# Performance work log

Hardware: AMD Instinct MI355X
Metric: run time of the kernel (lower is better)

## Reference

```python
import jax, jax.numpy as jnp
import numpy as np

HEADS = 8
SCALE_BASE = 512
EPS = 1e-5


def xpos(x, downscale=False):
    # x: (B, h, S, hd) ; XPOS rotary embedding with exponential scale
    hd = x.shape[-1]
    S = x.shape[-2]
    half = hd // 2
    base_scale = (jnp.arange(0, hd, 2, dtype=jnp.float32) + 0.4 * hd) / (1.4 * hd)  # (half,)
    pos = jnp.arange(S, dtype=jnp.float32)
    scale = base_scale[None, :] ** (pos[:, None] / SCALE_BASE)  # (S, half)
    inv_freq = 1.0 / (10000.0 ** (jnp.arange(half, dtype=jnp.float32) / half))
    sinu = pos[:, None] * inv_freq[None, :]  # (S, half)
    sin, cos = jnp.sin(sinu), jnp.cos(sinu)
    if downscale:
        scale = 1.0 / scale
    # duplicate_interleave: (S, half) -> (S, hd)
    sin_s = jnp.repeat(sin * scale, 2, axis=-1)
    cos_s = jnp.repeat(cos * scale, 2, axis=-1)
    x1 = x[..., ::2]
    x2 = x[..., 1::2]
    rot = jnp.stack((-x2, x1), axis=-1).reshape(x.shape)  # rotate_every_two
    return x * cos_s + rot * sin_s


def decay_mask(S):
    # (heads, S, S): gamma^(n-m) for n>=m else 0
    gammas = 1.0 - jnp.exp(jnp.linspace(np.log(1 / 32), np.log(1 / 512), HEADS)).astype(jnp.float32)
    n = jnp.arange(S, dtype=jnp.float32)
    diff = n[:, None] - n[None, :]
    lg = jnp.log(gammas)[:, None, None]
    return jnp.where(diff >= 0, jnp.exp(jnp.maximum(diff, 0.0) * lg), 0.0)


def layer_norm(x, w, b):
    mu = x.mean(-1, keepdims=True)
    var = x.var(-1, keepdims=True)
    return (x - mu) / jnp.sqrt(var + EPS) * w + b


def multiscale_retention(Xq, Xkv, Wq, Wk, Wv, Wg, Wo, gn_w, gn_b):
    # Xq: (B,S,d) query source; Xkv: (B,S,d) key/value source (== Xq for self)
    B, S, _ = Xq.shape
    Q = jnp.einsum('bsd,hde->bhse', Xq, Wq)
    K = jnp.einsum('btd,hde->bhte', Xkv, Wk)
    V = jnp.einsum('btd,hdv->bhtv', Xkv, Wv)
    Q = xpos(Q)
    K = xpos(K, downscale=True)
    D = decay_mask(S)  # (h,S,S)
    scores = jnp.einsum('bhse,bhte->bhst', Q, K) * D[None]
    Y = jnp.einsum('bhst,bhtv->bhsv', scores, V)  # (B,h,S,hv)
    h, hv = Y.shape[1], Y.shape[3]
    # GroupNorm(heads, v_dim) over each head's channels per token
    mu = Y.mean(-1, keepdims=True)
    var = Y.var(-1, keepdims=True)
    Yn = (Y - mu) / jnp.sqrt(var + EPS)
    Yn = Yn.transpose(0, 2, 1, 3).reshape(B, S, h * hv) * gn_w + gn_b
    gate = jax.nn.sigmoid(Xq @ Wg) * (Xq @ Wg)  # swish gate
    return (gate * Yn) @ Wo


def setup_inputs() -> dict:
    key = jax.random.key(0)
    ks = jax.random.split(key, 32)
    d, f, h, hd, hv, vd = 1024, 4096, 8, 128, 256, 2048
    B, S = 2, 2048
    inp = {
        'X': jax.random.normal(ks[0], (B, S, d), jnp.float32),
        'mem': jax.random.normal(ks[1], (B, S, d), jnp.float32),
        'ln1_w': jax.random.uniform(ks[2], (d,), jnp.float32, 0.5, 1.5),
        'ln1_b': jax.random.normal(ks[3], (d,), jnp.float32) * 0.1,
        'ln2_w': jax.random.uniform(ks[4], (d,), jnp.float32, 0.5, 1.5),
        'ln2_b': jax.random.normal(ks[5], (d,), jnp.float32) * 0.1,
        'Wq': jax.random.normal(ks[6], (h, d, hd), jnp.float32) / d,
        'Wk': jax.random.normal(ks[7], (h, d, hd), jnp.float32) / d,
        'Wv': jax.random.normal(ks[8], (h, d, hv), jnp.float32) / d,
        'Wg': jax.random.normal(ks[9], (d, vd), jnp.float32) / d,
        'Wo': jax.random.normal(ks[10], (vd, d), jnp.float32) / d,
        'gn_w': jax.random.uniform(ks[11], (vd,), jnp.float32, 0.5, 1.5),
        'gn_b': jax.random.normal(ks[12], (vd,), jnp.float32) * 0.1,
        'cWq': jax.random.normal(ks[13], (h, d, hd), jnp.float32) / d,
        'cWk': jax.random.normal(ks[14], (h, d, hd), jnp.float32) / d,
        'cWv': jax.random.normal(ks[15], (h, d, hv), jnp.float32) / d,
        'cWg': jax.random.normal(ks[16], (d, vd), jnp.float32) / d,
        'cWo': jax.random.normal(ks[17], (vd, d), jnp.float32) / d,
        'cgn_w': jax.random.uniform(ks[18], (vd,), jnp.float32, 0.5, 1.5),
        'cgn_b': jax.random.normal(ks[19], (vd,), jnp.float32) * 0.1,
        'W1': jax.random.normal(ks[20], (d, f), jnp.float32) * (1.0 / np.sqrt(d)),
        'b1': jax.random.normal(ks[21], (f,), jnp.float32) * 0.02,
        'W2': jax.random.normal(ks[22], (f, d), jnp.float32) * (1.0 / np.sqrt(f)),
        'b2': jax.random.normal(ks[23], (d,), jnp.float32) * 0.02,
    }
    return inp


def reference(X, mem, ln1_w, ln1_b, ln2_w, ln2_b, Wq, Wk, Wv, Wg, Wo, gn_w, gn_b,
              cWq, cWk, cWv, cWg, cWo, cgn_w, cgn_b, W1, b1, W2, b2):
    # self retention block
    X = multiscale_retention(layer_norm(X, ln1_w, ln1_b), None, Wq, Wk, Wv, Wg, Wo, gn_w, gn_b) + X if False else multiscale_retention(layer_norm(X, ln1_w, ln1_b), layer_norm(X, ln1_w, ln1_b), Wq, Wk, Wv, Wg, Wo, gn_w, gn_b) + X
    # cross retention block (note: original reuses layer_norms_2 for both this and the FFN)
    h2 = layer_norm(X, ln2_w, ln2_b)
    X = multiscale_retention(h2, mem, cWq, cWk, cWv, cWg, cWo, cgn_w, cgn_b) + X
    # FFN block (GELU exact, per torch nn.GELU default)
    h3 = layer_norm(X, ln2_w, ln2_b)
    X = (jax.nn.gelu(h3 @ W1 + b1, approximate=False) @ W2 + b2) + X
    return X
```

## Files before the change

kernel.cpp:

```cpp
#include <hip/hip_runtime.h>
#include <math.h>

#define RTOT 4096
#define SEQQ 2048

typedef unsigned int uint32;
typedef __attribute__((ext_vector_type(4))) float f32x4;
typedef __attribute__((ext_vector_type(8))) short bf16x8;

__device__ __forceinline__ unsigned short f2bf(float f) {
  unsigned int u = __float_as_uint(f);
  u = (u + 0x7FFFu + ((u >> 16) & 1u)) >> 16;
  return (unsigned short)u;
}
__device__ __forceinline__ float bf2f(unsigned short h) {
  return __uint_as_float(((unsigned int)h) << 16);
}
__device__ __forceinline__ void gld16(const void* g, void* l) {
  __builtin_amdgcn_global_load_lds(
      (const __attribute__((address_space(1))) uint32*)g,
      (__attribute__((address_space(3))) uint32*)l, 16, 0, 0);
}
__device__ __forceinline__ void bar() {
  asm volatile("" ::: "memory");
  __builtin_amdgcn_s_barrier();
  asm volatile("" ::: "memory");
}
#define VMCNT(n) asm volatile("s_waitcnt vmcnt(" #n ")" ::: "memory")

__global__ __launch_bounds__(256) void transpose_bf16(
    const float* __restrict__ in, unsigned short* __restrict__ out, int R, int C,
    int perm) {
  __shared__ float t[32][33];
  int z = blockIdx.z;
  in  += (size_t)z * R * C;
  out += (size_t)z * C * R;
  int r0 = blockIdx.x * 32, c0 = blockIdx.y * 32;
  int tx = threadIdx.x & 31, ty = threadIdx.x >> 5;
  #pragma unroll
  for (int i = 0; i < 4; ++i) {
    int r = ty + i * 8;
    t[r][tx] = in[(size_t)(r0 + r) * C + c0 + tx];
  }
  __syncthreads();
  #pragma unroll
  for (int i = 0; i < 4; ++i) {
    int cc = c0 + ty + i * 8;
    if (perm) cc = 64 * (cc >> 6) + ((cc & 1) << 5) + ((cc & 63) >> 1);
    out[(size_t)cc * R + r0 + tx] = f2bf(t[tx][ty + i * 8]);
  }
}

__global__ __launch_bounds__(256) void cvt_bf16(
    const float* __restrict__ in, unsigned short* __restrict__ out, int n8) {
  int i = blockIdx.x * 256 + threadIdx.x;
  if (i >= n8) return;
  const float4* p = (const float4*)(in + (size_t)i * 8);
  float4 a = p[0], b = p[1];
  bf16x8 v;
  v[0] = (short)f2bf(a.x); v[1] = (short)f2bf(a.y); v[2] = (short)f2bf(a.z); v[3] = (short)f2bf(a.w);
  v[4] = (short)f2bf(b.x); v[5] = (short)f2bf(b.y); v[6] = (short)f2bf(b.z); v[7] = (short)f2bf(b.w);
  *(bf16x8*)(out + (size_t)i * 8) = v;
}

__global__ __launch_bounds__(256) void tabgen(float* __restrict__ tab) {
  int i = blockIdx.x * 256 + threadIdx.x;
  int pos = i >> 6, j = i & 63;
  float bs = (2.f * (float)j + 51.2f) * (1.f / 179.2f);
  float e = (float)pos * (1.f / 512.f);
  float sc = exp2f(e * log2f(bs));
  float invf = exp2f(-(float)j * (13.287712379549449f / 64.f));
  float su, cu;
  sincosf((float)pos * invf, &su, &cu);
  tab[i]            = cu * sc;
  tab[131072 + i]   = su * sc;
  float si = 1.f / sc;
  tab[262144 + i]   = cu * si;
  tab[393216 + i]   = su * si;
}

__global__ __launch_bounds__(256) void ln_bf16(const float* __restrict__ x,
    const float* __restrict__ w, const float* __restrict__ b,
    unsigned short* __restrict__ out) {
  int row = blockIdx.x, tid = threadIdx.x;
  const float* xr = x + (size_t)row * 1024;
  float4 v = *(const float4*)(xr + tid * 4);
  float s  = v.x + v.y + v.z + v.w;
  float ss = v.x*v.x + v.y*v.y + v.z*v.z + v.w*v.w;
  #pragma unroll
  for (int o = 32; o > 0; o >>= 1) { s += __shfl_down(s, o); ss += __shfl_down(ss, o); }
  __shared__ float red[2][4];
  int wid = tid >> 6;
  if ((tid & 63) == 0) { red[0][wid] = s; red[1][wid] = ss; }
  __syncthreads();
  float st  = red[0][0] + red[0][1] + red[0][2] + red[0][3];
  float sst = red[1][0] + red[1][1] + red[1][2] + red[1][3];
  float mu   = st * (1.f / 1024.f);
  float var  = sst * (1.f / 1024.f) - mu * mu;
  float rstd = rsqrtf(var + 1e-5f);
  float4 wv = *(const float4*)(w + tid * 4);
  float4 bv = *(const float4*)(b + tid * 4);
  unsigned short o0 = f2bf((v.x - mu) * rstd * wv.x + bv.x);
  unsigned short o1 = f2bf((v.y - mu) * rstd * wv.y + bv.y);
  unsigned short o2 = f2bf((v.z - mu) * rstd * wv.z + bv.z);
  unsigned short o3 = f2bf((v.w - mu) * rstd * wv.w + bv.w);
  ushort4 o4 = make_ushort4(o0, o1, o2, o3);
  *(ushort4*)(out + (size_t)row * 1024 + tid * 4) = o4;
}

enum { EPI_F32_RES = 0, EPI_BF16 = 1, EPI_XPOS = 2, EPI_GELU = 4, EPI_BRES = 5,
       EPI_QKG = 6, EPI_QG = 7 };

struct EpiP {
  void* C; int ldc;
  const float* bias; const float* resid;
  const float* tab;
  unsigned short* oQ; unsigned short* oK; unsigned short* oG;
};

template<int EPI>
__device__ __forceinline__ void epi_store(size_t m, int n, int N0, float v, const EpiP& P) {
  if constexpr (EPI == EPI_BF16) {
    ((unsigned short*)P.C)[m * P.ldc + n] = f2bf(v);
  } else if constexpr (EPI == EPI_GELU) {
    v += P.bias[n];
    v = 0.5f * v * (1.f + erff(v * 0.70710678f));
    ((unsigned short*)P.C)[m * P.ldc + n] = f2bf(v);
  } else if constexpr (EPI == EPI_BRES) {
    v += P.bias[n] + P.resid[m * P.ldc + n];
    ((float*)P.C)[m * P.ldc + n] = v;
  } else {
    v += P.resid[m * P.ldc + n];
    ((float*)P.C)[m * P.ldc + n] = v;
  }
}

template<int EPI>
__global__ __launch_bounds__(256) void gemm_mfma(
    const unsigned short* __restrict__ A, int lda,
    const unsigned short* __restrict__ Bt, int ldb, int K, EpiP P) {
  __shared__ __align__(16) unsigned short As[3][128 * 32];
  __shared__ __align__(16) unsigned short Bs[3][128 * 32];
  const int tid = threadIdx.x, w = tid >> 6, lane = tid & 63;
  const int M0 = blockIdx.y * 128, N0 = blockIdx.x * 128;
  const int fr = lane & 15, fs = lane >> 4;
  const int srow = lane >> 2, sp = lane & 3;

  f32x4 zf = {0.f, 0.f, 0.f, 0.f};
  f32x4 acc[4][4];
  #pragma unroll
  for (int i = 0; i < 4; ++i)
    #pragma unroll
    for (int j = 0; j < 4; ++j) acc[i][j] = zf;

  auto STAGE = [&](int buf, int k0) {
    #pragma unroll
    for (int c = 0; c < 4; ++c) {
      int ch = w * 4 + c;
      int cc = ch & 7;
      int row = cc * 16 + srow;
      int so = sp ^ ((row >> 1) & 3);
      if (ch < 8) gld16(A  + (size_t)(M0 + row) * lda + k0 + so * 8, &As[buf][cc * 512]);
      else        gld16(Bt + (size_t)(N0 + row) * ldb + k0 + so * 8, &Bs[buf][cc * 512]);
    }
  };

  const int NT = K >> 5;
  STAGE(0, 0);
  STAGE(1, 32);
  int cur = 0, sb = 1;
  for (int t = 0; t < NT; ++t) {
    if (t + 2 < NT)      { sb = (sb == 2) ? 0 : sb + 1; STAGE(sb, (t + 2) * 32); VMCNT(8); }
    else if (t + 1 < NT) { VMCNT(4); }
    else                 { VMCNT(0); }
    bar();
    bf16x8 af[4], bfr[4];
    #pragma unroll
    for (int mi = 0; mi < 4; ++mi) {
      int row = (w >> 1) * 64 + mi * 16 + fr;
      af[mi] = *(const bf16x8*)(&As[cur][row * 32 + (fs ^ ((row >> 1) & 3)) * 8]);
    }
    #pragma unroll
    for (int ni = 0; ni < 4; ++ni) {
      int row = (w & 1) * 64 + ni * 16 + fr;
      bfr[ni] = *(const bf16x8*)(&Bs[cur][row * 32 + (fs ^ ((row >> 1) & 3)) * 8]);
    }
    #pragma unroll
    for (int mi = 0; mi < 4; ++mi)
      #pragma unroll
      for (int ni = 0; ni < 4; ++ni)
        acc[mi][ni] = __builtin_amdgcn_mfma_f32_16x16x32_bf16(af[mi], bfr[ni], acc[mi][ni], 0, 0, 0);
    bar();
    cur = (cur == 2) ? 0 : cur + 1;
  }

  #pragma unroll
  for (int mi = 0; mi < 4; ++mi)
    #pragma unroll
    for (int r = 0; r < 4; ++r) {
      size_t m = M0 + (w >> 1) * 64 + mi * 16 + fs * 4 + r;
      #pragma unroll
      for (int ni = 0; ni < 4; ++ni) {
        int n = N0 + (w & 1) * 64 + ni * 16 + fr;
        epi_store<EPI>(m, n, N0, acc[mi][ni][r], P);
      }
    }
}

template<int EPI>
__global__ __launch_bounds__(256) void gemm_bn64(
    const unsigned short* __restrict__ A, int lda,
    const unsigned short* __restrict__ Bt, int ldb, int K, EpiP P) {
  __shared__ __align__(16) unsigned short As[3][128 * 32];
  __shared__ __align__(16) unsigned short Bs[3][64 * 32];
  const int tid = threadIdx.x, w = tid >> 6, lane = tid & 63;
  const int M0 = blockIdx.y * 128, N0 = blockIdx.x * 64;
  const int fr = lane & 15, fs = lane >> 4;
  const int srow = lane >> 2, sp = lane & 3;

  f32x4 zf = {0.f, 0.f, 0.f, 0.f};
  f32x4 acc[2][4];
  #pragma unroll
  for (int i = 0; i < 2; ++i)
    #pragma unroll
    for (int j = 0; j < 4; ++j) acc[i][j] = zf;

  auto STAGE = [&](int buf, int k0) {
    #pragma unroll
    for (int c = 0; c < 3; ++c) {
      int ch = w * 3 + c;
      if (ch < 8) {
        int row = ch * 16 + srow;
        int so = sp ^ ((row >> 1) & 3);
        gld16(A + (size_t)(M0 + row) * lda + k0 + so * 8, &As[buf][ch * 512]);
      } else {
        int bch = ch - 8;
        int row = bch * 16 + srow;
        int so = sp ^ ((row >> 1) & 3);
        gld16(Bt + (size_t)(N0 + row) * ldb + k0 + so * 8, &Bs[buf][bch * 512]);
      }
    }
  };

  const int NT = K >> 5;
  STAGE(0, 0);
  STAGE(1, 32);
  int cur = 0, sb = 1;
  for (int t = 0; t < NT; ++t) {
    if (t + 2 < NT)      { sb = (sb == 2) ? 0 : sb + 1; STAGE(sb, (t + 2) * 32); VMCNT(6); }
    else if (t + 1 < NT) { VMCNT(3); }
    else                 { VMCNT(0); }
    bar();
    bf16x8 af[2], bfr[4];
    #pragma unroll
    for (int mi = 0; mi < 2; ++mi) {
      int row = w * 32 + mi * 16 + fr;
      af[mi] = *(const bf16x8*)(&As[cur][row * 32 + (fs ^ ((row >> 1) & 3)) * 8]);
    }
    #pragma unroll
    for (int ni = 0; ni < 4; ++ni) {
      int row = ni * 16 + fr;
      bfr[ni] = *(const bf16x8*)(&Bs[cur][row * 32 + (fs ^ ((row >> 1) & 3)) * 8]);
    }
    #pragma unroll
    for (int mi = 0; mi < 2; ++mi)
      #pragma unroll
      for (int ni = 0; ni < 4; ++ni)
        acc[mi][ni] = __builtin_amdgcn_mfma_f32_16x16x32_bf16(af[mi], bfr[ni], acc[mi][ni], 0, 0, 0);
    bar();
    cur = (cur == 2) ? 0 : cur + 1;
  }

  if constexpr (EPI == EPI_XPOS) {
    int gsel = (N0 >> 6) & 1;
    #pragma unroll
    for (int mi = 0; mi < 2; ++mi)
      #pragma unroll
      for (int r = 0; r < 4; ++r) {
        size_t m = M0 + w * 32 + mi * 16 + fs * 4 + r;
        int pos = (int)(m & (SEQQ - 1));
        #pragma unroll
        for (int ni = 0; ni < 2; ++ni) {
          int j = gsel * 32 + ni * 16 + fr;
          float cs = P.tab[pos * 64 + j], sn = P.tab[131072 + pos * 64 + j];
          float ve = acc[mi][ni][r], vo = acc[mi][ni + 2][r];
          unsigned short* dst = (unsigned short*)P.C;
          dst[m * P.ldc + N0 + ni * 16 + fr]       = f2bf(ve * cs - vo * sn);
          dst[m * P.ldc + N0 + (ni + 2) * 16 + fr] = f2bf(vo * cs + ve * sn);
        }
      }
  } else {
    #pragma unroll
    for (int mi = 0; mi < 2; ++mi)
      #pragma unroll
      for (int r = 0; r < 4; ++r) {
        size_t m = M0 + w * 32 + mi * 16 + fs * 4 + r;
        #pragma unroll
        for (int ni = 0; ni < 4; ++ni) {
          int n = N0 + ni * 16 + fr;
          epi_store<EPI>(m, n, N0, acc[mi][ni][r], P);
        }
      }
  }
}

template<int EPI>
__global__ __launch_bounds__(512, 2) void gemm256(
    const unsigned short* __restrict__ A,
    const unsigned short* __restrict__ Bt,
    int nbx, EpiP P) {
  __shared__ __align__(16) unsigned short lds[4][2][8192];
  const int tid = threadIdx.x, w = tid >> 6, lane = tid & 63;
  int cpx = (int)gridDim.x >> 3;
  int sbid = ((int)blockIdx.x & 7) * cpx + ((int)blockIdx.x >> 3);
  int by = sbid / nbx, bx = sbid - by * nbx;
  const int M0 = by * 256, N0 = bx * 256;
  const int wm = w >> 2, wn = w & 3;
  const int fr = lane & 15, fs = lane >> 4;
  const int srow = lane >> 2;
  const int sslot = (lane & 3) ^ ((lane >> 3) & 3);
  const int rsw = (fr >> 1) & 3;

  f32x4 acc[8][4];
  #pragma unroll
  for (int i = 0; i < 8; ++i)
    #pragma unroll
    for (int j = 0; j < 4; ++j) acc[i][j] = {0.f, 0.f, 0.f, 0.f};

  auto STAGE = [&](int t, int buf) {
    int k0 = t * 32;
    #pragma unroll
    for (int j = 0; j < 4; ++j) {
      int c = w * 4 + j;
      if (c < 16)
        gld16(A  + (size_t)(M0 + c * 16 + srow) * 1024 + k0 + sslot * 8,
              &lds[buf][0][c * 512]);
      else
        gld16(Bt + (size_t)(N0 + (c - 16) * 16 + srow) * 1024 + k0 + sslot * 8,
              &lds[buf][1][(c - 16) * 512]);
    }
  };
  auto COMPUTE = [&](int t) {
    const unsigned short* la = &lds[t & 3][0][wm * 128 * 32];
    const unsigned short* lb = &lds[t & 3][1][wn * 64 * 32];
    bf16x8 a[8], b[4];
    #pragma unroll
    for (int ni = 0; ni < 4; ++ni)
      b[ni] = *(const bf16x8*)(lb + (ni * 16 + fr) * 32 + ((fs ^ rsw) * 8));
    #pragma unroll
    for (int mi = 0; mi < 8; ++mi)
      a[mi] = *(const bf16x8*)(la + (mi * 16 + fr) * 32 + ((fs ^ rsw) * 8));
    #pragma unroll
    for (int mi = 0; mi < 8; ++mi)
      #pragma unroll
      for (int ni = 0; ni < 4; ++ni)
        acc[mi][ni] = __builtin_amdgcn_mfma_f32_16x16x32_bf16(a[mi], b[ni], acc[mi][ni], 0, 0, 0);
  };

  STAGE(0, 0); STAGE(1, 1); STAGE(2, 2);
  for (int t = 0; t < 29; ++t) {
    STAGE(t + 3, (t + 3) & 3);
    VMCNT(12);
    bar();
    COMPUTE(t);
    bar();
  }
  VMCNT(8);  bar(); COMPUTE(29); bar();
  VMCNT(4);  bar(); COMPUTE(30); bar();
  VMCNT(0);  bar(); COMPUTE(31);

  if constexpr (EPI == EPI_GELU) {
    #pragma unroll
    for (int mi = 0; mi < 8; ++mi)
      #pragma unroll
      for (int r = 0; r < 4; ++r) {
        size_t m = M0 + wm * 128 + mi * 16 + fs * 4 + r;
        #pragma unroll
        for (int ni = 0; ni < 4; ++ni) {
          int n = N0 + wn * 64 + ni * 16 + fr;
          float v = acc[mi][ni][r] + P.bias[n];
          v = 0.5f * v * (1.f + erff(v * 0.70710678f));
          ((unsigned short*)P.C)[m * P.ldc + n] = f2bf(v);
        }
      }
  } else {
    const int nb = N0 + wn * 64;
    const bool isQ = nb < 1024;
    const bool isK = (EPI == EPI_QKG) && !isQ && (nb < 2048);
    if (isQ || isK) {
      const float* tc = isK ? P.tab + 262144 : P.tab;
      const float* ts = tc + 131072;
      unsigned short* dst = isK ? P.oK : P.oQ;
      const int nloc = isK ? nb - 1024 : nb;
      const int gsel = (nloc >> 6) & 1;
      #pragma unroll
      for (int mi = 0; mi < 8; ++mi)
        #pragma unroll
        for (int r = 0; r < 4; ++r) {
          size_t m = M0 + wm * 128 + mi * 16 + fs * 4 + r;
          int pos = (int)(m & (SEQQ - 1));
          #pragma unroll
          for (int ni = 0; ni < 2; ++ni) {
            int j = gsel * 32 + ni * 16 + fr;
            float cs = tc[pos * 64 + j], sn = ts[pos * 64 + j];
            float ve = acc[mi][ni][r], vo = acc[mi][ni + 2][r];
            dst[m * 1024 + nloc + ni * 16 + fr]       = f2bf(ve * cs - vo * sn);
            dst[m * 1024 + nloc + (ni + 2) * 16 + fr] = f2bf(vo * cs + ve * sn);
          }
        }
    } else {
      const int nloc = nb - ((EPI == EPI_QKG) ? 2048 : 1024);
      #pragma unroll
      for (int mi = 0; mi < 8; ++mi)
        #pragma unroll
        for (int r = 0; r < 4; ++r) {
          size_t m = M0 + wm * 128 + mi * 16 + fs * 4 + r;
          #pragma unroll
          for (int ni = 0; ni < 4; ++ni) {
            float v = acc[mi][ni][r];
            P.oG[m * 2048 + nloc + ni * 16 + fr] = f2bf(v / (1.f + expf(-v)));
          }
        }
    }
  }
}

__global__ __launch_bounds__(256) void retention_mfma(
    const unsigned short* __restrict__ Qx, const unsigned short* __restrict__ Kx,
    const unsigned short* __restrict__ VT, const unsigned short* __restrict__ Gate,
    const float* __restrict__ gnw, const float* __restrict__ gnb,
    unsigned short* __restrict__ Gout) {
  __shared__ __align__(16) unsigned short Ks[2][32 * 128];
  __shared__ __align__(16) unsigned short Vs[2][256 * 32];
  const int tid = threadIdx.x, w = tid >> 6, lane = tid & 63;
  int bid = blockIdx.x, qt, h, b;
  if (bid < 256) { qt = 31 - (bid >> 3); h = bid & 7; b = 0; }
  else           { int k = bid - 256; qt = k >> 3; h = k & 7; b = 1; }
  const int q0 = qt * 64;
  const int fr = lane & 15, fs = lane >> 4;

  float gamma = 1.f - expf(-3.4657359028f - 0.3960841032f * (float)h);
  float l2g = log2f(gamma);
  const int qglob = q0 + w * 16 + fr;

  size_t qrow = (size_t)b * SEQQ + qglob;
  bf16x8 qf[4];
  #pragma unroll
  for (int ks = 0; ks < 4; ++ks)
    qf[ks] = *(const bf16x8*)(Qx + qrow * 1024 + h * 128 + ks * 32 + fs * 8);

  float gtl8[8];
  #pragma unroll
  for (int i = 0; i < 8; ++i) {
    int toff = (i >> 2) * 16 + fs * 4 + (i & 3);
    gtl8[i] = exp2f(-(float)toff * l2g);
  }

  f32x4 zf = {0.f, 0.f, 0.f, 0.f};
  f32x4 yacc[16];
  #pragma unroll
  for (int i = 0; i < 16; ++i) yacc[i] = zf;

  int cutoff = (int)(27.f / (-l2g));
  int t_start = q0 - cutoff;
  if (t_start < 0) t_start = 0;
  t_start &= ~31;
  size_t kbase = (size_t)b * SEQQ;

  auto STAGE = [&](int buf, int t0) {
    #pragma unroll
    for (int c = 0; c < 2; ++c) {
      int ch = w * 2 + c;
      int row = ch * 4 + (lane >> 4);
      int so = (lane & 15) ^ (row & 15);
      gld16(Kx + (kbase + t0 + row) * 1024 + h * 128 + so * 8, &Ks[buf][ch * 512]);
    }
    #pragma unroll
    for (int c = 0; c < 4; ++c) {
      int ch = w * 4 + c;
      int vrow = ch * 16 + (lane >> 2);
      int so = (lane & 3) ^ ((vrow >> 1) & 3);
      gld16(VT + (size_t)(h * 256 + vrow) * RTOT + kbase + t0 + so * 8, &Vs[buf][ch * 512]);
    }
  };

  STAGE(0, t_start);
  int cur = 0;
  for (int t0 = t_start; t0 < q0 + 64; t0 += 32) {
    if (t0 + 32 < q0 + 64) { STAGE(cur ^ 1, t0 + 32); VMCNT(6); }
    else                   { VMCNT(0); }
    bar();

    f32x4 sacc[2];
    sacc[0] = zf; sacc[1] = zf;
    #pragma unroll
    for (int nt = 0; nt < 2; ++nt) {
      int row = nt * 16 + fr;
      #pragma unroll
      for (int ks = 0; ks < 4; ++ks) {
        int sl = ks * 4 + fs;
        bf16x8 kf = *(const bf16x8*)(&Ks[cur][row * 128 + (sl ^ (row & 15)) * 8]);
        sacc[nt] = __builtin_amdgcn_mfma_f32_16x16x32_bf16(kf, qf[ks], sacc[nt], 0, 0, 0);
      }
    }
    float fsc = exp2f((float)(qglob - t0) * l2g);
    uint32 pk[4];
    #pragma unroll
    for (int nt = 0; nt < 2; ++nt)
      #pragma unroll
      for (int hf = 0; hf < 2; ++hf) {
        int r0i = hf * 2;
        int ta = t0 + nt * 16 + fs * 4 + r0i;
        float va = (qglob >= ta)     ? sacc[nt][r0i]     * (fsc * gtl8[nt * 4 + r0i])     : 0.f;
        float vb = (qglob >= ta + 1) ? sacc[nt][r0i + 1] * (fsc * gtl8[nt * 4 + r0i + 1]) : 0.f;
        pk[nt * 2 + hf] = (uint32)f2bf(va) | ((uint32)f2bf(vb) << 16);
      }
    union { uint32 u[4]; bf16x8 v8; } pa;
    #pragma unroll
    for (int j = 0; j < 4; ++j) {
      int src = fr + 16 * (2 * (fs & 1) + (j >> 1));
      int v0 = __shfl((int)pk[j & 1],     src);
      int v1 = __shfl((int)pk[2 + (j & 1)], src);
      pa.u[j] = (fs < 2) ? (uint32)v0 : (uint32)v1;
    }
    #pragma unroll
    for (int nv = 0; nv < 16; ++nv) {
      int vrow = nv * 16 + fr;
      bf16x8 vf = *(const bf16x8*)(&Vs[cur][vrow * 32 + (fs ^ ((vrow >> 1) & 3)) * 8]);
      yacc[nv] = __builtin_amdgcn_mfma_f32_16x16x32_bf16(pa.v8, vf, yacc[nv], 0, 0, 0);
    }
    bar();
    cur ^= 1;
  }

  #pragma unroll
  for (int r = 0; r < 4; ++r) {
    float s = 0.f, sq = 0.f;
    #pragma unroll
    for (int nv = 0; nv < 16; ++nv) { float v = yacc[nv][r]; s += v; sq += v * v; }
    #pragma unroll
    for (int msk = 1; msk < 16; msk <<= 1) { s += __shfl_xor(s, msk); sq += __shfl_xor(sq, msk); }
    float mu = s * (1.f / 256.f);
    float var = sq * (1.f / 256.f) - mu * mu;
    float rstd = rsqrtf(var + 1e-5f);
    int srow = q0 + w * 16 + fs * 4 + r;
    size_t mrow = (size_t)b * SEQQ + srow;
    const unsigned short* grow = Gate + mrow * 2048 + h * 256;
    unsigned short* orow = Gout + mrow * 2048 + h * 256;
    #pragma unroll
    for (int nv = 0; nv < 16; ++nv) {
      int col = nv * 16 + fr;
      float yn = (yacc[nv][r] - mu) * rstd * gnw[h * 256 + col] + gnb[h * 256 + col];
      orow[col] = f2bf(bf2f(grow[col]) * yn);
    }
  }
}

extern "C" void kernel_launch(void* const* d_in, const int* in_sizes, int n_in,
                              void* d_out, int out_size, void* d_ws, size_t ws_size,
                              hipStream_t stream) {
  const float* X    = (const float*)d_in[0];
  const float* mem  = (const float*)d_in[1];
  const float* ln1w = (const float*)d_in[2];
  const float* ln1b = (const float*)d_in[3];
  const float* ln2w = (const float*)d_in[4];
  const float* ln2b = (const float*)d_in[5];
  const float* Wq   = (const float*)d_in[6];
  const float* Wk   = (const float*)d_in[7];
  const float* Wv   = (const float*)d_in[8];
  const float* Wg   = (const float*)d_in[9];
  const float* Wo   = (const float*)d_in[10];
  const float* gnw  = (const float*)d_in[11];
  const float* gnb  = (const float*)d_in[12];
  const float* cWq  = (const float*)d_in[13];
  const float* cWk  = (const float*)d_in[14];
  const float* cWv  = (const float*)d_in[15];
  const float* cWg  = (const float*)d_in[16];
  const float* cWo  = (const float*)d_in[17];
  const float* cgnw = (const float*)d_in[18];
  const float* cgnb = (const float*)d_in[19];
  const float* W1   = (const float*)d_in[20];
  const float* b1   = (const float*)d_in[21];
  const float* W2   = (const float*)d_in[22];
  const float* b2   = (const float*)d_in[23];
  float* out = (float*)d_out;

  const size_t MB = 1024ull * 1024ull;
  if (ws_size < 106 * MB) return;
  unsigned char* W8 = (unsigned char*)d_ws;
  unsigned short* WqkgT = (unsigned short*)(W8 + 0 * MB);
  unsigned short* WvT   = (unsigned short*)(W8 + 8 * MB);
  unsigned short* WoT   = (unsigned short*)(W8 + 12 * MB);
  unsigned short* cQGT  = (unsigned short*)(W8 + 16 * MB);
  unsigned short* cWkT  = (unsigned short*)(W8 + 22 * MB);
  unsigned short* cWvT  = (unsigned short*)(W8 + 24 * MB);
  unsigned short* cWoT  = (unsigned short*)(W8 + 28 * MB);
  float*          tab   = (float*)(W8 + 32 * MB);
  unsigned short* hbuf  = (unsigned short*)(W8 + 34 * MB);
  unsigned short* Qx    = (unsigned short*)(W8 + 42 * MB);
  unsigned short* Kx    = (unsigned short*)(W8 + 50 * MB);
  unsigned short* W1T   = Qx;
  unsigned short* W2T   = Kx;
  unsigned short* VTb   = (unsigned short*)(W8 + 58 * MB);
  unsigned short* Gg    = (unsigned short*)(W8 + 74 * MB);
  unsigned short* Tb    = VTb;
  unsigned short* GoutB = (unsigned short*)(W8 + 90 * MB);
  unsigned short* mem16 = GoutB;

  transpose_bf16<<<dim3(32, 4, 8),  256, 0, stream>>>(Wq,  WqkgT,               1024, 128, 1);
  transpose_bf16<<<dim3(32, 4, 8),  256, 0, stream>>>(Wk,  WqkgT + 1024 * 1024, 1024, 128, 1);
  transpose_bf16<<<dim3(32, 64, 1), 256, 0, stream>>>(Wg,  WqkgT + 2048 * 1024, 1024, 2048, 0);
  transpose_bf16<<<dim3(32, 8, 8),  256, 0, stream>>>(Wv,  WvT,  1024, 256, 0);
  transpose_bf16<<<dim3(64, 32, 1), 256, 0, stream>>>(Wo,  WoT,  2048, 1024, 0);
  transpose_bf16<<<dim3(32, 4, 8),  256, 0, stream>>>(cWq, cQGT,               1024, 128, 1);
  transpose_bf16<<<dim3(32, 64, 1), 256, 0, stream>>>(cWg, cQGT + 1024 * 1024, 1024, 2048, 0);
  transpose_bf16<<<dim3(32, 4, 8),  256, 0, stream>>>(cWk, cWkT, 1024, 128, 1);
  transpose_bf16<<<dim3(32, 8, 8),  256, 0, stream>>>(cWv, cWvT, 1024, 256, 0);
  transpose_bf16<<<dim3(64, 32, 1), 256, 0, stream>>>(cWo, cWoT, 2048, 1024, 0);
  tabgen<<<512, 256, 0, stream>>>(tab);

  EpiP P{};

  ln_bf16<<<RTOT, 256, 0, stream>>>(X, ln1w, ln1b, hbuf);
  P = EpiP{nullptr, 0, nullptr, nullptr, tab, Qx, Kx, Gg};
  gemm256<EPI_QKG><<<256, 512, 0, stream>>>(hbuf, WqkgT, 16, P);
  P = EpiP{VTb, 4096, nullptr, nullptr, nullptr, nullptr, nullptr, nullptr};
  gemm_mfma<EPI_BF16><<<dim3(32, 16), 256, 0, stream>>>(WvT, 1024, hbuf, 1024, 1024, P);
  retention_mfma<<<dim3(512), 256, 0, stream>>>(Qx, Kx, VTb, Gg, gnw, gnb, GoutB);
  P = EpiP{out, 1024, nullptr, X, nullptr, nullptr, nullptr, nullptr};
  gemm_bn64<EPI_F32_RES><<<dim3(16, 32), 256, 0, stream>>>(GoutB, 2048, WoT, 2048, 2048, P);

  cvt_bf16<<<2048, 256, 0, stream>>>(mem, mem16, 524288);
  ln_bf16<<<RTOT, 256, 0, stream>>>(out, ln2w, ln2b, hbuf);
  P = EpiP{nullptr, 0, nullptr, nullptr, tab, Qx, nullptr, Gg};
  gemm256<EPI_QG><<<192, 512, 0, stream>>>(hbuf, cQGT, 12, P);
  P = EpiP{Kx, 1024, nullptr, nullptr, tab + 262144, nullptr, nullptr, nullptr};
  gemm_bn64<EPI_XPOS><<<dim3(16, 32), 256, 0, stream>>>(mem16, 1024, cWkT, 1024, 1024, P);
  P = EpiP{VTb, 4096, nullptr, nullptr, nullptr, nullptr, nullptr, nullptr};
  gemm_mfma<EPI_BF16><<<dim3(32, 16), 256, 0, stream>>>(cWvT, 1024, mem16, 1024, 1024, P);
  retention_mfma<<<dim3(512), 256, 0, stream>>>(Qx, Kx, VTb, Gg, cgnw, cgnb, GoutB);
  P = EpiP{out, 1024, nullptr, out, nullptr, nullptr, nullptr, nullptr};
  gemm_bn64<EPI_F32_RES><<<dim3(16, 32), 256, 0, stream>>>(GoutB, 2048, cWoT, 2048, 2048, P);

  transpose_bf16<<<dim3(32, 128, 1), 256, 0, stream>>>(W1, W1T, 1024, 4096, 0);
  transpose_bf16<<<dim3(128, 32, 1), 256, 0, stream>>>(W2, W2T, 4096, 1024, 0);
  ln_bf16<<<RTOT, 256, 0, stream>>>(out, ln2w, ln2b, hbuf);
  P = EpiP{Tb, 4096, b1, nullptr, nullptr, nullptr, nullptr, nullptr};
  gemm256<EPI_GELU><<<256, 512, 0, stream>>>(hbuf, W1T, 16, P);
  P = EpiP{out, 1024, b2, out, nullptr, nullptr, nullptr, nullptr};
  gemm_bn64<EPI_BRES><<<dim3(16, 32), 256, 0, stream>>>(Tb, 4096, W2T, 4096, 4096, P);
}
```

Before: 589.1 us.

## Split GEMM k-steps into two halves interleaving prefetch with MFMA and raise priority

Measured after the change: 598.6 us. About the same (+1.6%).

```diff
diff --git a/kernel.cpp b/kernel.cpp
--- a/kernel.cpp
+++ b/kernel.cpp
@@ -153,9 +153,9 @@
     #pragma unroll
     for (int j = 0; j < 4; ++j) acc[i][j] = zf;
 
-  auto STAGE = [&](int buf, int k0) {
-    #pragma unroll
-    for (int c = 0; c < 4; ++c) {
+  auto STAGE2 = [&](int buf, int k0, int half) {
+    #pragma unroll
+    for (int c = half * 2; c < half * 2 + 2; ++c) {
       int ch = w * 4 + c;
       int cc = ch & 7;
       int row = cc * 16 + srow;
@@ -166,30 +166,47 @@
   };
 
   const int NT = K >> 5;
-  STAGE(0, 0);
-  STAGE(1, 32);
+  STAGE2(0, 0, 0);  STAGE2(0, 0, 1);
+  STAGE2(1, 32, 0); STAGE2(1, 32, 1);
   int cur = 0, sb = 1;
   for (int t = 0; t < NT; ++t) {
-    if (t + 2 < NT)      { sb = (sb == 2) ? 0 : sb + 1; STAGE(sb, (t + 2) * 32); VMCNT(8); }
+    bool more = (t + 2 < NT);
+    if (more)            { sb = (sb == 2) ? 0 : sb + 1; STAGE2(sb, (t + 2) * 32, 0); VMCNT(6); }
     else if (t + 1 < NT) { VMCNT(4); }
     else                 { VMCNT(0); }
     bar();
-    bf16x8 af[4], bfr[4];
-    #pragma unroll
-    for (int mi = 0; mi < 4; ++mi) {
-      int row = (w >> 1) * 64 + mi * 16 + fr;
-      af[mi] = *(const bf16x8*)(&As[cur][row * 32 + (fs ^ ((row >> 1) & 3)) * 8]);
-    }
+    bf16x8 bfr[4], af[2];
     #pragma unroll
     for (int ni = 0; ni < 4; ++ni) {
       int row = (w & 1) * 64 + ni * 16 + fr;
       bfr[ni] = *(const bf16x8*)(&Bs[cur][row * 32 + (fs ^ ((row >> 1) & 3)) * 8]);
     }
     #pragma unroll
-    for (int mi = 0; mi < 4; ++mi)
+    for (int mi = 0; mi < 2; ++mi) {
+      int row = (w >> 1) * 64 + mi * 16 + fr;
+      af[mi] = *(const bf16x8*)(&As[cur][row * 32 + (fs ^ ((row >> 1) & 3)) * 8]);
+    }
+    __builtin_amdgcn_s_setprio(1);
+    #pragma unroll
+    for (int mi = 0; mi < 2; ++mi)
       #pragma unroll
       for (int ni = 0; ni < 4; ++ni)
         acc[mi][ni] = __builtin_amdgcn_mfma_f32_16x16x32_bf16(af[mi], bfr[ni], acc[mi][ni], 0, 0, 0);
+    __builtin_amdgcn_s_setprio(0);
+    bar();
+    if (more) STAGE2(sb, (t + 2) * 32, 1);
+    #pragma unroll
+    for (int mi = 0; mi < 2; ++mi) {
+      int row = (w >> 1) * 64 + (mi + 2) * 16 + fr;
+      af[mi] = *(const bf16x8*)(&As[cur][row * 32 + (fs ^ ((row >> 1) & 3)) * 8]);
+    }
+    __builtin_amdgcn_s_setprio(1);
+    #pragma unroll
+    for (int mi = 0; mi < 2; ++mi)
+      #pragma unroll
+      for (int ni = 0; ni < 4; ++ni)
+        acc[mi + 2][ni] = __builtin_amdgcn_mfma_f32_16x16x32_bf16(af[mi], bfr[ni], acc[mi + 2][ni], 0, 0, 0);
+    __builtin_amdgcn_s_setprio(0);
     bar();
     cur = (cur == 2) ? 0 : cur + 1;
   }
@@ -262,11 +279,13 @@
       int row = ni * 16 + fr;
       bfr[ni] = *(const bf16x8*)(&Bs[cur][row * 32 + (fs ^ ((row >> 1) & 3)) * 8]);
     }
+    __builtin_amdgcn_s_setprio(1);
     #pragma unroll
     for (int mi = 0; mi < 2; ++mi)
       #pragma unroll
       for (int ni = 0; ni < 4; ++ni)
         acc[mi][ni] = __builtin_amdgcn_mfma_f32_16x16x32_bf16(af[mi], bfr[ni], acc[mi][ni], 0, 0, 0);
+    __builtin_amdgcn_s_setprio(0);
     bar();
     cur = (cur == 2) ? 0 : cur + 1;
   }
@@ -327,10 +346,10 @@
     #pragma unroll
     for (int j = 0; j < 4; ++j) acc[i][j] = {0.f, 0.f, 0.f, 0.f};
 
-  auto STAGE = [&](int t, int buf) {
+  auto STAGE2 = [&](int t, int buf, int half) {
     int k0 = t * 32;
     #pragma unroll
-    for (int j = 0; j < 4; ++j) {
+    for (int j = half * 2; j < half * 2 + 2; ++j) {
       int c = w * 4 + j;
       if (c < 16)
         gld16(A  + (size_t)(M0 + c * 16 + srow) * 1024 + k0 + sslot * 8,
@@ -340,34 +359,46 @@
               &lds[buf][1][(c - 16) * 512]);
     }
   };
-  auto COMPUTE = [&](int t) {
+
+  bf16x8 bq[4], aq[4];
+  auto LOADB = [&](int t) {
+    const unsigned short* lb = &lds[t & 3][1][wn * 64 * 32];
+    #pragma unroll
+    for (int ni = 0; ni < 4; ++ni)
+      bq[ni] = *(const bf16x8*)(lb + (ni * 16 + fr) * 32 + ((fs ^ rsw) * 8));
+  };
+  auto LOADA = [&](int t, int h) {
     const unsigned short* la = &lds[t & 3][0][wm * 128 * 32];
-    const unsigned short* lb = &lds[t & 3][1][wn * 64 * 32];
-    bf16x8 a[8], b[4];
-    #pragma unroll
-    for (int ni = 0; ni < 4; ++ni)
-      b[ni] = *(const bf16x8*)(lb + (ni * 16 + fr) * 32 + ((fs ^ rsw) * 8));
-    #pragma unroll
-    for (int mi = 0; mi < 8; ++mi)
-      a[mi] = *(const bf16x8*)(la + (mi * 16 + fr) * 32 + ((fs ^ rsw) * 8));
-    #pragma unroll
-    for (int mi = 0; mi < 8; ++mi)
+    #pragma unroll
+    for (int mi = 0; mi < 4; ++mi)
+      aq[mi] = *(const bf16x8*)(la + ((h * 4 + mi) * 16 + fr) * 32 + ((fs ^ rsw) * 8));
+  };
+  auto MM = [&](int h) {
+    __builtin_amdgcn_s_setprio(1);
+    #pragma unroll
+    for (int mi = 0; mi < 4; ++mi)
       #pragma unroll
       for (int ni = 0; ni < 4; ++ni)
-        acc[mi][ni] = __builtin_amdgcn_mfma_f32_16x16x32_bf16(a[mi], b[ni], acc[mi][ni], 0, 0, 0);
+        acc[h * 4 + mi][ni] = __builtin_amdgcn_mfma_f32_16x16x32_bf16(aq[mi], bq[ni], acc[h * 4 + mi][ni], 0, 0, 0);
+    __builtin_amdgcn_s_setprio(0);
   };
 
-  STAGE(0, 0); STAGE(1, 1); STAGE(2, 2);
+  STAGE2(0, 0, 0); STAGE2(0, 0, 1);
+  STAGE2(1, 1, 0); STAGE2(1, 1, 1);
+  STAGE2(2, 2, 0); STAGE2(2, 2, 1);
   for (int t = 0; t < 29; ++t) {
-    STAGE(t + 3, (t + 3) & 3);
-    VMCNT(12);
-    bar();
-    COMPUTE(t);
-    bar();
-  }
-  VMCNT(8);  bar(); COMPUTE(29); bar();
-  VMCNT(4);  bar(); COMPUTE(30); bar();
-  VMCNT(0);  bar(); COMPUTE(31);
+    STAGE2(t + 3, (t + 3) & 3, 0);
+    VMCNT(10);
+    bar();
+    LOADB(t); LOADA(t, 0); MM(0);
+    bar();
+    STAGE2(t + 3, (t + 3) & 3, 1);
+    LOADA(t, 1); MM(1);
+    bar();
+  }
+  VMCNT(8); bar(); LOADB(29); LOADA(29, 0); MM(0); bar(); LOADA(29, 1); MM(1); bar();
+  VMCNT(4); bar(); LOADB(30); LOADA(30, 0); MM(0); bar(); LOADA(30, 1); MM(1); bar();
+  VMCNT(0); bar(); LOADB(31); LOADA(31, 0); MM(0); bar(); LOADA(31, 1); MM(1);
 
   if constexpr (EPI == EPI_GELU) {
     #pragma unroll
```

## Use XCD-aware block swizzle and double-buffered LDS in the 128-row GEMMs

Applied to the files above, without the earlier changes.

Result: faster. 570.6 us (-3.1%).

```diff
diff --git a/kernel.cpp b/kernel.cpp
--- a/kernel.cpp
+++ b/kernel.cpp
@@ -138,11 +138,14 @@
 template<int EPI>
 __global__ __launch_bounds__(256) void gemm_mfma(
     const unsigned short* __restrict__ A, int lda,
-    const unsigned short* __restrict__ Bt, int ldb, int K, EpiP P) {
-  __shared__ __align__(16) unsigned short As[3][128 * 32];
-  __shared__ __align__(16) unsigned short Bs[3][128 * 32];
+    const unsigned short* __restrict__ Bt, int ldb, int K, int nbx, EpiP P) {
+  __shared__ __align__(16) unsigned short As[2][128 * 32];
+  __shared__ __align__(16) unsigned short Bs[2][128 * 32];
   const int tid = threadIdx.x, w = tid >> 6, lane = tid & 63;
-  const int M0 = blockIdx.y * 128, N0 = blockIdx.x * 128;
+  int q8 = (int)gridDim.x >> 3;
+  int sbid = ((int)blockIdx.x & 7) * q8 + ((int)blockIdx.x >> 3);
+  int by = sbid / nbx, bx = sbid - by * nbx;
+  const int M0 = by * 128, N0 = bx * 128;
   const int fr = lane & 15, fs = lane >> 4;
   const int srow = lane >> 2, sp = lane & 3;
 
@@ -165,14 +168,11 @@
     }
   };
 
-  const int NT = K >> 5;
   STAGE(0, 0);
-  STAGE(1, 32);
-  int cur = 0, sb = 1;
-  for (int t = 0; t < NT; ++t) {
-    if (t + 2 < NT)      { sb = (sb == 2) ? 0 : sb + 1; STAGE(sb, (t + 2) * 32); VMCNT(8); }
-    else if (t + 1 < NT) { VMCNT(4); }
-    else                 { VMCNT(0); }
+  int cur = 0;
+  for (int k0 = 0; k0 < K; k0 += 32) {
+    if (k0 + 32 < K) { STAGE(cur ^ 1, k0 + 32); VMCNT(4); }
+    else             { VMCNT(0); }
     bar();
     bf16x8 af[4], bfr[4];
     #pragma unroll
@@ -191,7 +191,7 @@
       for (int ni = 0; ni < 4; ++ni)
         acc[mi][ni] = __builtin_amdgcn_mfma_f32_16x16x32_bf16(af[mi], bfr[ni], acc[mi][ni], 0, 0, 0);
     bar();
-    cur = (cur == 2) ? 0 : cur + 1;
+    cur ^= 1;
   }
 
   #pragma unroll
@@ -210,11 +210,14 @@
 template<int EPI>
 __global__ __launch_bounds__(256) void gemm_bn64(
     const unsigned short* __restrict__ A, int lda,
-    const unsigned short* __restrict__ Bt, int ldb, int K, EpiP P) {
-  __shared__ __align__(16) unsigned short As[3][128 * 32];
-  __shared__ __align__(16) unsigned short Bs[3][64 * 32];
+    const unsigned short* __restrict__ Bt, int ldb, int K, int nbx, EpiP P) {
+  __shared__ __align__(16) unsigned short As[2][128 * 32];
+  __shared__ __align__(16) unsigned short Bs[2][64 * 32];
   const int tid = threadIdx.x, w = tid >> 6, lane = tid & 63;
-  const int M0 = blockIdx.y * 128, N0 = blockIdx.x * 64;
+  int q8 = (int)gridDim.x >> 3;
+  int sbid = ((int)blockIdx.x & 7) * q8 + ((int)blockIdx.x >> 3);
+  int by = sbid / nbx, bx = sbid - by * nbx;
+  const int M0 = by * 128, N0 = bx * 64;
   const int fr = lane & 15, fs = lane >> 4;
   const int srow = lane >> 2, sp = lane & 3;
 
@@ -242,14 +245,11 @@
     }
   };
 
-  const int NT = K >> 5;
   STAGE(0, 0);
-  STAGE(1, 32);
-  int cur = 0, sb = 1;
-  for (int t = 0; t < NT; ++t) {
-    if (t + 2 < NT)      { sb = (sb == 2) ? 0 : sb + 1; STAGE(sb, (t + 2) * 32); VMCNT(6); }
-    else if (t + 1 < NT) { VMCNT(3); }
-    else                 { VMCNT(0); }
+  int cur = 0;
+  for (int k0 = 0; k0 < K; k0 += 32) {
+    if (k0 + 32 < K) { STAGE(cur ^ 1, k0 + 32); VMCNT(3); }
+    else             { VMCNT(0); }
     bar();
     bf16x8 af[2], bfr[4];
     #pragma unroll
@@ -268,7 +268,7 @@
       for (int ni = 0; ni < 4; ++ni)
         acc[mi][ni] = __builtin_amdgcn_mfma_f32_16x16x32_bf16(af[mi], bfr[ni], acc[mi][ni], 0, 0, 0);
     bar();
-    cur = (cur == 2) ? 0 : cur + 1;
+    cur ^= 1;
   }
 
   if constexpr (EPI == EPI_XPOS) {
@@ -625,22 +625,22 @@
   P = EpiP{nullptr, 0, nullptr, nullptr, tab, Qx, Kx, Gg};
   gemm256<EPI_QKG><<<256, 512, 0, stream>>>(hbuf, WqkgT, 16, P);
   P = EpiP{VTb, 4096, nullptr, nullptr, nullptr, nullptr, nullptr, nullptr};
-  gemm_mfma<EPI_BF16><<<dim3(32, 16), 256, 0, stream>>>(WvT, 1024, hbuf, 1024, 1024, P);
+  gemm_mfma<EPI_BF16><<<512, 256, 0, stream>>>(WvT, 1024, hbuf, 1024, 1024, 32, P);
   retention_mfma<<<dim3(512), 256, 0, stream>>>(Qx, Kx, VTb, Gg, gnw, gnb, GoutB);
   P = EpiP{out, 1024, nullptr, X, nullptr, nullptr, nullptr, nullptr};
-  gemm_bn64<EPI_F32_RES><<<dim3(16, 32), 256, 0, stream>>>(GoutB, 2048, WoT, 2048, 2048, P);
+  gemm_bn64<EPI_F32_RES><<<512, 256, 0, stream>>>(GoutB, 2048, WoT, 2048, 2048, 16, P);
 
   cvt_bf16<<<2048, 256, 0, stream>>>(mem, mem16, 524288);
   ln_bf16<<<RTOT, 256, 0, stream>>>(out, ln2w, ln2b, hbuf);
   P = EpiP{nullptr, 0, nullptr, nullptr, tab, Qx, nullptr, Gg};
   gemm256<EPI_QG><<<192, 512, 0, stream>>>(hbuf, cQGT, 12, P);
   P = EpiP{Kx, 1024, nullptr, nullptr, tab + 262144, nullptr, nullptr, nullptr};
-  gemm_bn64<EPI_XPOS><<<dim3(16, 32), 256, 0, stream>>>(mem16, 1024, cWkT, 1024, 1024, P);
+  gemm_bn64<EPI_XPOS><<<512, 256, 0, stream>>>(mem16, 1024, cWkT, 1024, 1024, 16, P);
   P = EpiP{VTb, 4096, nullptr, nullptr, nullptr, nullptr, nullptr, nullptr};
-  gemm_mfma<EPI_BF16><<<dim3(32, 16), 256, 0, stream>>>(cWvT, 1024, mem16, 1024, 1024, P);
+  gemm_mfma<EPI_BF16><<<512, 256, 0, stream>>>(cWvT, 1024, mem16, 1024, 1024, 32, P);
   retention_mfma<<<dim3(512), 256, 0, stream>>>(Qx, Kx, VTb, Gg, cgnw, cgnb, GoutB);
   P = EpiP{out, 1024, nullptr, out, nullptr, nullptr, nullptr, nullptr};
-  gemm_bn64<EPI_F32_RES><<<dim3(16, 32), 256, 0, stream>>>(GoutB, 2048, cWoT, 2048, 2048, P);
+  gemm_bn64<EPI_F32_RES><<<512, 256, 0, stream>>>(GoutB, 2048, cWoT, 2048, 2048, 16, P);
 
   transpose_bf16<<<dim3(32, 128, 1), 256, 0, stream>>>(W1, W1T, 1024, 4096, 0);
   transpose_bf16<<<dim3(128, 32, 1), 256, 0, stream>>>(W2, W2T, 4096, 1024, 0);
@@ -648,5 +648,5 @@
   P = EpiP{Tb, 4096, b1, nullptr, nullptr, nullptr, nullptr, nullptr};
   gemm256<EPI_GELU><<<256, 512, 0, stream>>>(hbuf, W1T, 16, P);
   P = EpiP{out, 1024, b2, out, nullptr, nullptr, nullptr, nullptr};
-  gemm_bn64<EPI_BRES><<<dim3(16, 32), 256, 0, stream>>>(Tb, 4096, W2T, 4096, 4096, P);
-}
+  gemm_bn64<EPI_BRES><<<512, 256, 0, stream>>>(Tb, 4096, W2T, 4096, 4096, 16, P);
+}
```
